# Performance work log

Measured on AMD Instinct MI355X. Metric: run time of the kernel, lower is better.

The kernel has to match this reference:

```python
import jax, jax.numpy as jnp
import numpy as np
from jax import lax

D_MODEL = 512
D_STATE = 16
D_CONV = 4
EXPAND = 2
D_INNER = EXPAND * D_MODEL          # 1024
DT_RANK = int(np.ceil(D_MODEL / 16))  # 32


def setup_inputs() -> dict:
    key = jax.random.key(0)
    ks = jax.random.split(key, 10)
    s = lambda k, shape, sc: (jax.random.normal(k, shape, dtype=jnp.float32) * sc)
    x = jax.random.normal(ks[0], (8, D_MODEL, 128, 128), dtype=jnp.float32)
    W_in = s(ks[1], (2 * D_INNER, D_MODEL), 1.0 / np.sqrt(D_MODEL))
    conv_w = s(ks[2], (D_INNER, D_CONV), 1.0 / np.sqrt(D_CONV))
    conv_b = s(ks[3], (D_INNER,), 0.02)
    W_x = s(ks[4], (DT_RANK + 2 * D_STATE, D_INNER), 1.0 / np.sqrt(D_INNER))
    W_dt = s(ks[5], (D_INNER, DT_RANK), 1.0 / np.sqrt(DT_RANK))
    b_dt = s(ks[6], (D_INNER,), 0.02)
    # S4D-real init: A_log[d, n] = log(n+1)
    A_log = jnp.log(jnp.broadcast_to(jnp.arange(1, D_STATE + 1, dtype=jnp.float32), (D_INNER, D_STATE)))
    D_param = jnp.ones((D_INNER,), dtype=jnp.float32)
    W_out = s(ks[7], (D_MODEL, D_INNER), 1.0 / np.sqrt(D_INNER))
    return {"x": x, "W_in": W_in, "conv_w": conv_w, "conv_b": conv_b,
            "W_x": W_x, "W_dt": W_dt, "b_dt": b_dt, "A_log": A_log,
            "D_param": D_param, "W_out": W_out}


def _mamba(u, W_in, conv_w, conv_b, W_x, W_dt, b_dt, A_log, D_param, W_out):
    # u: (B, L, D_MODEL)
    B, L, _ = u.shape
    xz = jnp.einsum('bld,ed->ble', u, W_in)          # (B, L, 2*D_INNER)
    xp, z = jnp.split(xz, 2, axis=-1)                # each (B, L, D_INNER)
    # causal depthwise conv1d over L
    xc = lax.conv_general_dilated(
        xp.transpose(0, 2, 1), conv_w[:, None, :],
        window_strides=(1,), padding=((D_CONV - 1, 0),),
        dimension_numbers=('NCH', 'OIH', 'NCH'),
        feature_group_count=D_INNER)
    xc = xc[:, :, :L] + conv_b[None, :, None]
    xs = jax.nn.silu(xc.transpose(0, 2, 1))          # (B, L, D_INNER)
    x_dbl = jnp.einsum('bld,ed->ble', xs, W_x)       # (B, L, DT_RANK+2*D_STATE)
    dt, Bm, Cm = jnp.split(x_dbl, [DT_RANK, DT_RANK + D_STATE], axis=-1)
    delta = jax.nn.softplus(jnp.einsum('blr,dr->bld', dt, W_dt) + b_dt)  # (B,L,D_INNER)
    A = -jnp.exp(A_log)                              # (D_INNER, D_STATE)
    dA = jnp.exp(jnp.einsum('bld,dn->bldn', delta, A))
    dBx = jnp.einsum('bld,bln,bld->bldn', delta, Bm, xs)

    def step(h, inp):
        dA_t, dBx_t, C_t = inp
        h = dA_t * h + dBx_t                         # (B, D_INNER, D_STATE)
        y = jnp.einsum('bdn,bn->bd', h, C_t)
        return h, y

    h0 = jnp.zeros((B, D_INNER, D_STATE), dtype=u.dtype)
    _, ys = lax.scan(step, h0, (dA.transpose(1, 0, 2, 3),
                                dBx.transpose(1, 0, 2, 3),
                                Cm.transpose(1, 0, 2)))
    y = ys.transpose(1, 0, 2)                        # (B, L, D_INNER)
    y = y + D_param * xs
    y = y * jax.nn.silu(z)
    return jnp.einsum('bld,ed->ble', y, W_out)       # (B, L, D_MODEL)


def reference(x, W_in, conv_w, conv_b, W_x, W_dt, b_dt, A_log, D_param, W_out):
    # ECA: global avg pool -> (B, 1, C) sequence through Mamba -> sigmoid gate
    y = jnp.mean(x, axis=(2, 3))[:, None, :]         # (B, 1, C)
    y = _mamba(y, W_in, conv_w, conv_b, W_x, W_dt, b_dt, A_log, D_param, W_out)
    gate = jax.nn.sigmoid(y)[:, 0, :, None, None]    # (B, C, 1, 1)
    return x * gate
```

## Files before the change

### kernel.cpp

```cpp
#include <hip/hip_runtime.h>
#include <math.h>

#define DMODEL 512
#define DINNER 1024
#define DTRANK 32
#define DSTATE 16
#define HW     16384
#define BATCH  8

typedef float vf4 __attribute__((ext_vector_type(4)));

__device__ __forceinline__ float wave_reduce(float s) {
#pragma unroll
    for (int off = 32; off; off >>= 1) s += __shfl_xor(s, off);
    return s;
}

__global__ __launch_bounds__(256) void mean_kernel(const float* __restrict__ x,
                                                   float* __restrict__ mean_out) {
    const int row = blockIdx.x;
    const vf4* xr = (const vf4*)(x + (size_t)row * HW);
    const int t = threadIdx.x;
    float s = 0.f;
#pragma unroll
    for (int j = 0; j < 16; ++j) {
        vf4 v = xr[t + j * 256];
        s += v.x + v.y + v.z + v.w;
    }
    for (int off = 32; off; off >>= 1) s += __shfl_down(s, off);
    __shared__ float part[4];
    if ((t & 63) == 0) part[t >> 6] = s;
    __syncthreads();
    if (t == 0) {
        float tot = part[0] + part[1] + part[2] + part[3];
        mean_out[row] = tot * (1.0f / (float)HW);
    }
}

__global__ __launch_bounds__(256) void k2a_win_kernel(
    const float* __restrict__ mean_in,
    const float* __restrict__ W_in,
    const float* __restrict__ conv_w,
    const float* __restrict__ conv_b,
    float* __restrict__ xs_buf,
    float* __restrict__ sz_buf)
{
    __shared__ float u[BATCH * DMODEL];
    const int t = threadIdx.x;
#pragma unroll
    for (int i = 0; i < 16; ++i) u[t + i * 256] = mean_in[t + i * 256];
    __syncthreads();

    const int wave = blockIdx.x * 4 + (t >> 6);
    const int lane = t & 63;
    const vf4* row = (const vf4*)(W_in + (size_t)wave * DMODEL);
    const vf4 w0 = row[lane];
    const vf4 w1 = row[lane + 64];
    const vf4* u4 = (const vf4*)u;

    float acc[BATCH];
#pragma unroll
    for (int b = 0; b < BATCH; ++b) {
        vf4 a = u4[b * 128 + lane];
        vf4 c = u4[b * 128 + lane + 64];
        acc[b] = w0.x * a.x + w0.y * a.y + w0.z * a.z + w0.w * a.w
               + w1.x * c.x + w1.y * c.y + w1.z * c.z + w1.w * c.w;
    }
#pragma unroll
    for (int b = 0; b < BATCH; ++b) acc[b] = wave_reduce(acc[b]);

    if (lane == 0) {
        if (wave < DINNER) {
            const float cw = conv_w[wave * 4 + 3];
            const float cb = conv_b[wave];
#pragma unroll
            for (int b = 0; b < BATCH; ++b) {
                float xc = acc[b] * cw + cb;
                xs_buf[b * DINNER + wave] = xc / (1.f + expf(-xc));
            }
        } else {
            const int d = wave - DINNER;
#pragma unroll
            for (int b = 0; b < BATCH; ++b) {
                float zc = acc[b];
                sz_buf[b * DINNER + d] = zc / (1.f + expf(-zc));
            }
        }
    }
}

__global__ __launch_bounds__(256) void k2b_mid_kernel(
    const float* __restrict__ xs_buf,
    const float* __restrict__ sz_buf,
    const float* __restrict__ W_x,
    const float* __restrict__ W_dt,
    const float* __restrict__ b_dt,
    const float* __restrict__ D_param,
    float* __restrict__ yv_buf)
{
    __shared__ float xs[DINNER];
    __shared__ float xdbl[64];
    const int b = blockIdx.x;
    const int t = threadIdx.x;
    const int lane = t & 63;
    const int wv = t >> 6;

#pragma unroll
    for (int i = 0; i < 4; ++i) xs[t + i * 256] = xs_buf[b * DINNER + t + i * 256];
    __syncthreads();

    const vf4* xs4 = (const vf4*)xs;
    for (int oi = 0; oi < 16; ++oi) {
        const int o = wv * 16 + oi;
        const vf4* wr = (const vf4*)(W_x + (size_t)o * DINNER);
        float acc = 0.f;
#pragma unroll
        for (int j = 0; j < 4; ++j) {
            vf4 w = wr[lane + j * 64];
            vf4 v = xs4[lane + j * 64];
            acc += w.x * v.x + w.y * v.y + w.z * v.z + w.w * v.w;
        }
        acc = wave_reduce(acc);
        if (lane == 0) xdbl[o] = acc;
    }
    __syncthreads();

    float bc = 0.f;
#pragma unroll
    for (int n = 0; n < DSTATE; ++n)
        bc += xdbl[DTRANK + n] * xdbl[DTRANK + DSTATE + n];

#pragma unroll
    for (int k = 0; k < 4; ++k) {
        const int d = t + k * 256;
        float acc = b_dt[d];
        const vf4* wr = (const vf4*)(W_dt + (size_t)d * DTRANK);
        const vf4* dt4 = (const vf4*)xdbl;
#pragma unroll
        for (int r = 0; r < 8; ++r) {
            vf4 w = wr[r]; vf4 v = dt4[r];
            acc += w.x * v.x + w.y * v.y + w.z * v.z + w.w * v.w;
        }
        float delta = (acc > 20.f) ? acc : log1pf(expf(acc));
        yv_buf[b * DINNER + d] =
            (delta * bc + D_param[d]) * xs[d] * sz_buf[b * DINNER + d];
    }
}

__global__ __launch_bounds__(256) void gate_mul_kernel(
    const float* __restrict__ x,
    const float* __restrict__ yv_buf,
    const float* __restrict__ W_out,
    float* __restrict__ out)
{
    const int row = (BATCH * DMODEL - 1) - blockIdx.x;
    const int b = row >> 9;
    const int c = row & 511;
    const int t = threadIdx.x;
    const int lane = t & 63;

    const vf4* wr = (const vf4*)(W_out + (size_t)c * DINNER);
    const vf4* yv = (const vf4*)(yv_buf + (size_t)b * DINNER);
    vf4 w[4], y[4];
#pragma unroll
    for (int j = 0; j < 4; ++j) { w[j] = wr[lane + j * 64]; y[j] = yv[lane + j * 64]; }

    const vf4* xi = (const vf4*)(x + (size_t)row * HW);
    vf4* oo = (vf4*)(out + (size_t)row * HW);
    vf4 v[16];
#pragma unroll
    for (int j = 0; j < 16; ++j) v[j] = xi[t + j * 256];

    float acc = 0.f;
#pragma unroll
    for (int j = 0; j < 4; ++j)
        acc += w[j].x * y[j].x + w[j].y * y[j].y + w[j].z * y[j].z + w[j].w * y[j].w;
    acc = wave_reduce(acc);
    const float g = 1.f / (1.f + expf(-acc));

#pragma unroll
    for (int j = 0; j < 16; ++j) {
        vf4 o = v[j] * g;
        __builtin_nontemporal_store(o, &oo[t + j * 256]);
    }
}

extern "C" void kernel_launch(void* const* d_in, const int* in_sizes, int n_in,
                              void* d_out, int out_size, void* d_ws, size_t ws_size,
                              hipStream_t stream) {
    const float* x       = (const float*)d_in[0];
    const float* W_in    = (const float*)d_in[1];
    const float* conv_w  = (const float*)d_in[2];
    const float* conv_b  = (const float*)d_in[3];
    const float* W_x     = (const float*)d_in[4];
    const float* W_dt    = (const float*)d_in[5];
    const float* b_dt    = (const float*)d_in[6];
    const float* D_param = (const float*)d_in[8];
    const float* W_out   = (const float*)d_in[9];
    float* out = (float*)d_out;

    float* mean_buf = (float*)d_ws;
    float* xs_buf   = mean_buf + BATCH * DMODEL;
    float* sz_buf   = xs_buf + BATCH * DINNER;
    float* yv_buf   = sz_buf + BATCH * DINNER;

    mean_kernel<<<BATCH * DMODEL, 256, 0, stream>>>(x, mean_buf);
    k2a_win_kernel<<<512, 256, 0, stream>>>(mean_buf, W_in, conv_w, conv_b,
                                            xs_buf, sz_buf);
    k2b_mid_kernel<<<BATCH, 256, 0, stream>>>(xs_buf, sz_buf, W_x, W_dt, b_dt,
                                              D_param, yv_buf);
    gate_mul_kernel<<<BATCH * DMODEL, 256, 0, stream>>>(x, yv_buf, W_out, out);
}
```

Measured before the change: 149.0 us.

## Repartition Mamba matvec kernels across more blocks and reorder gate loads

The W_in projection kernel now uses one block per output row, with each wave handling two batches and reading mean values straight from global memory instead of staging them in shared memory. The mid kernel moves to 512 threads per block, and the gate kernel computes its dot product before streaming x, with a partial unroll and an occupancy hint of 6 in launch bounds. The goal is more parallelism in the small matvec kernels and lower register pressure in the bandwidth-bound gate kernel. The risk is that the gate kernel loses its up-front load of all x values, which gave memory-level parallelism.

Measured after the change: 144.5 us, median of 2. 1.03x faster.

```diff
diff --git a/kernel.cpp b/kernel.cpp
--- a/kernel.cpp
+++ b/kernel.cpp
@@ -14,6 +14,10 @@
 #pragma unroll
     for (int off = 32; off; off >>= 1) s += __shfl_xor(s, off);
     return s;
+}
+
+__device__ __forceinline__ float dot4(vf4 a, vf4 b) {
+    return a.x * b.x + a.y * b.y + a.z * b.z + a.w * b.w;
 }
 
 __global__ __launch_bounds__(256) void mean_kernel(const float* __restrict__ x,
@@ -45,51 +49,47 @@
     float* __restrict__ xs_buf,
     float* __restrict__ sz_buf)
 {
-    __shared__ float u[BATCH * DMODEL];
-    const int t = threadIdx.x;
-#pragma unroll
-    for (int i = 0; i < 16; ++i) u[t + i * 256] = mean_in[t + i * 256];
-    __syncthreads();
-
-    const int wave = blockIdx.x * 4 + (t >> 6);
+    const int e = blockIdx.x;
+    const int t = threadIdx.x;
     const int lane = t & 63;
-    const vf4* row = (const vf4*)(W_in + (size_t)wave * DMODEL);
+    const int wv = t >> 6;
+
+    const vf4* row = (const vf4*)(W_in + (size_t)e * DMODEL);
     const vf4 w0 = row[lane];
     const vf4 w1 = row[lane + 64];
-    const vf4* u4 = (const vf4*)u;
-
-    float acc[BATCH];
-#pragma unroll
-    for (int b = 0; b < BATCH; ++b) {
+    const vf4* u4 = (const vf4*)mean_in;
+
+    float acc[2];
+#pragma unroll
+    for (int k = 0; k < 2; ++k) {
+        const int b = wv * 2 + k;
         vf4 a = u4[b * 128 + lane];
         vf4 c = u4[b * 128 + lane + 64];
-        acc[b] = w0.x * a.x + w0.y * a.y + w0.z * a.z + w0.w * a.w
-               + w1.x * c.x + w1.y * c.y + w1.z * c.z + w1.w * c.w;
-    }
-#pragma unroll
-    for (int b = 0; b < BATCH; ++b) acc[b] = wave_reduce(acc[b]);
+        acc[k] = dot4(w0, a) + dot4(w1, c);
+        acc[k] = wave_reduce(acc[k]);
+    }
 
     if (lane == 0) {
-        if (wave < DINNER) {
-            const float cw = conv_w[wave * 4 + 3];
-            const float cb = conv_b[wave];
-#pragma unroll
-            for (int b = 0; b < BATCH; ++b) {
-                float xc = acc[b] * cw + cb;
-                xs_buf[b * DINNER + wave] = xc / (1.f + expf(-xc));
+        if (e < DINNER) {
+            const float cw = conv_w[e * 4 + 3];
+            const float cb = conv_b[e];
+#pragma unroll
+            for (int k = 0; k < 2; ++k) {
+                float xc = acc[k] * cw + cb;
+                xs_buf[(wv * 2 + k) * DINNER + e] = xc / (1.f + expf(-xc));
             }
         } else {
-            const int d = wave - DINNER;
-#pragma unroll
-            for (int b = 0; b < BATCH; ++b) {
-                float zc = acc[b];
-                sz_buf[b * DINNER + d] = zc / (1.f + expf(-zc));
+            const int d = e - DINNER;
+#pragma unroll
+            for (int k = 0; k < 2; ++k) {
+                float zc = acc[k];
+                sz_buf[(wv * 2 + k) * DINNER + d] = zc / (1.f + expf(-zc));
             }
         }
     }
 }
 
-__global__ __launch_bounds__(256) void k2b_mid_kernel(
+__global__ __launch_bounds__(512) void k2b_mid_kernel(
     const float* __restrict__ xs_buf,
     const float* __restrict__ sz_buf,
     const float* __restrict__ W_x,
@@ -106,20 +106,17 @@
     const int wv = t >> 6;
 
 #pragma unroll
-    for (int i = 0; i < 4; ++i) xs[t + i * 256] = xs_buf[b * DINNER + t + i * 256];
+    for (int i = 0; i < 2; ++i) xs[t + i * 512] = xs_buf[b * DINNER + t + i * 512];
     __syncthreads();
 
     const vf4* xs4 = (const vf4*)xs;
-    for (int oi = 0; oi < 16; ++oi) {
-        const int o = wv * 16 + oi;
+    for (int oi = 0; oi < 8; ++oi) {
+        const int o = wv * 8 + oi;
         const vf4* wr = (const vf4*)(W_x + (size_t)o * DINNER);
         float acc = 0.f;
 #pragma unroll
-        for (int j = 0; j < 4; ++j) {
-            vf4 w = wr[lane + j * 64];
-            vf4 v = xs4[lane + j * 64];
-            acc += w.x * v.x + w.y * v.y + w.z * v.z + w.w * v.w;
-        }
+        for (int j = 0; j < 4; ++j)
+            acc += dot4(wr[lane + j * 64], xs4[lane + j * 64]);
         acc = wave_reduce(acc);
         if (lane == 0) xdbl[o] = acc;
     }
@@ -131,23 +128,21 @@
         bc += xdbl[DTRANK + n] * xdbl[DTRANK + DSTATE + n];
 
 #pragma unroll
-    for (int k = 0; k < 4; ++k) {
-        const int d = t + k * 256;
+    for (int k = 0; k < 2; ++k) {
+        const int d = t + k * 512;
         float acc = b_dt[d];
         const vf4* wr = (const vf4*)(W_dt + (size_t)d * DTRANK);
         const vf4* dt4 = (const vf4*)xdbl;
 #pragma unroll
-        for (int r = 0; r < 8; ++r) {
-            vf4 w = wr[r]; vf4 v = dt4[r];
-            acc += w.x * v.x + w.y * v.y + w.z * v.z + w.w * v.w;
-        }
+        for (int r = 0; r < 8; ++r)
+            acc += dot4(wr[r], dt4[r]);
         float delta = (acc > 20.f) ? acc : log1pf(expf(acc));
         yv_buf[b * DINNER + d] =
             (delta * bc + D_param[d]) * xs[d] * sz_buf[b * DINNER + d];
     }
 }
 
-__global__ __launch_bounds__(256) void gate_mul_kernel(
+__global__ __launch_bounds__(256, 6) void gate_mul_kernel(
     const float* __restrict__ x,
     const float* __restrict__ yv_buf,
     const float* __restrict__ W_out,
@@ -161,27 +156,19 @@
 
     const vf4* wr = (const vf4*)(W_out + (size_t)c * DINNER);
     const vf4* yv = (const vf4*)(yv_buf + (size_t)b * DINNER);
-    vf4 w[4], y[4];
-#pragma unroll
-    for (int j = 0; j < 4; ++j) { w[j] = wr[lane + j * 64]; y[j] = yv[lane + j * 64]; }
+    float acc = 0.f;
+#pragma unroll
+    for (int j = 0; j < 4; ++j)
+        acc += dot4(wr[lane + j * 64], yv[lane + j * 64]);
+    acc = wave_reduce(acc);
+    const float g = 1.f / (1.f + expf(-acc));
 
     const vf4* xi = (const vf4*)(x + (size_t)row * HW);
     vf4* oo = (vf4*)(out + (size_t)row * HW);
-    vf4 v[16];
-#pragma unroll
-    for (int j = 0; j < 16; ++j) v[j] = xi[t + j * 256];
-
-    float acc = 0.f;
-#pragma unroll
-    for (int j = 0; j < 4; ++j)
-        acc += w[j].x * y[j].x + w[j].y * y[j].y + w[j].z * y[j].z + w[j].w * y[j].w;
-    acc = wave_reduce(acc);
-    const float g = 1.f / (1.f + expf(-acc));
-
-#pragma unroll
+#pragma unroll 4
     for (int j = 0; j < 16; ++j) {
-        vf4 o = v[j] * g;
-        __builtin_nontemporal_store(o, &oo[t + j * 256]);
+        vf4 v = xi[t + j * 256] * g;
+        __builtin_nontemporal_store(v, &oo[t + j * 256]);
     }
 }
 
@@ -205,9 +192,9 @@
     float* yv_buf   = sz_buf + BATCH * DINNER;
 
     mean_kernel<<<BATCH * DMODEL, 256, 0, stream>>>(x, mean_buf);
-    k2a_win_kernel<<<512, 256, 0, stream>>>(mean_buf, W_in, conv_w, conv_b,
-                                            xs_buf, sz_buf);
-    k2b_mid_kernel<<<BATCH, 256, 0, stream>>>(xs_buf, sz_buf, W_x, W_dt, b_dt,
+    k2a_win_kernel<<<2048, 256, 0, stream>>>(mean_buf, W_in, conv_w, conv_b,
+                                             xs_buf, sz_buf);
+    k2b_mid_kernel<<<BATCH, 512, 0, stream>>>(xs_buf, sz_buf, W_x, W_dt, b_dt,
                                               D_param, yv_buf);
     gate_mul_kernel<<<BATCH * DMODEL, 256, 0, stream>>>(x, yv_buf, W_out, out);
 }
```
